# Performance work log

Hardware: AMD Instinct MI355X
Metric: run time of the kernel (lower is better)

The kernel has to match this reference:

```python
import jax, jax.numpy as jnp
import numpy as np

C = 256
CQK = C // 8  # query/key channel dim from Conv3d(in, in//8, 1)


def setup_inputs() -> dict:
    key = jax.random.key(0)
    ks = jax.random.split(key, 8)
    B, D, H, W = 2, 16, 16, 16
    x = jax.random.normal(ks[0], (B, C, D, H, W), dtype=jnp.float32)
    s = 1.0 / np.sqrt(C)
    q_w = jax.random.normal(ks[1], (CQK, C), dtype=jnp.float32) * s
    q_b = jax.random.normal(ks[2], (CQK,), dtype=jnp.float32) * 0.01
    k_w = jax.random.normal(ks[3], (CQK, C), dtype=jnp.float32) * s
    k_b = jax.random.normal(ks[4], (CQK,), dtype=jnp.float32) * 0.01
    v_w = jax.random.normal(ks[5], (C, C), dtype=jnp.float32) * s
    v_b = jax.random.normal(ks[6], (C,), dtype=jnp.float32) * 0.01
    gamma = jax.random.normal(ks[7], (1,), dtype=jnp.float32)
    return {"x": x, "q_w": q_w, "q_b": q_b, "k_w": k_w, "k_b": k_b,
            "v_w": v_w, "v_b": v_b, "gamma": gamma}


def reference(x, q_w, q_b, k_w, k_b, v_w, v_b, gamma):
    B, Cc, D, H, W = x.shape
    N = D * H * W
    xf = x.reshape(B, Cc, N)  # [B, C, N]
    # 1x1x1 Conv3d == channel-mixing matmul
    q = jnp.einsum('oc,bcn->bon', q_w, xf) + q_b[None, :, None]  # [B, C/8, N]
    k = jnp.einsum('oc,bcn->bon', k_w, xf) + k_b[None, :, None]  # [B, C/8, N]
    v = jnp.einsum('oc,bcn->bon', v_w, xf) + v_b[None, :, None]  # [B, C, N]
    # attention[b, i, j] = sum_c q[b, c, i] * k[b, c, j]
    attn = jnp.einsum('bci,bcj->bij', q, k)  # [B, N, N]
    attn = jax.nn.softmax(attn, axis=-1)
    # out[b, c, i] = sum_j v[b, c, j] * attn[b, i, j]
    out = jnp.einsum('bcj,bij->bci', v, attn)  # [B, C, N]
    out = out.reshape(B, Cc, D, H, W)
    return gamma[0] * out + x
```

## Files before the change

kernel.cpp:

```cpp
#include <hip/hip_runtime.h>

#define C_DIM 256
#define CQK   32
#define N_DIM 4096
#define B_DIM 2

typedef __attribute__((ext_vector_type(8))) short bf16x8;
typedef __attribute__((ext_vector_type(4))) float f32x4;

__device__ __forceinline__ unsigned short f2bf(float f) {
    union { float f; unsigned u; } v; v.f = f;
    unsigned r = v.u + 0x7FFFu + ((v.u >> 16) & 1u);
    return (unsigned short)(r >> 16);
}
__device__ __forceinline__ unsigned pk2(float a, float b) {
    return (unsigned)f2bf(a) | ((unsigned)f2bf(b) << 16);
}
__device__ __forceinline__ unsigned pk2t(float a, float b) {
    union { float f; unsigned u; } ua, ub; ua.f = a; ub.f = b;
    return __builtin_amdgcn_perm(ub.u, ua.u, 0x07060302u);
}
#define EXP2(x) __builtin_amdgcn_exp2f(x)
#define MFMA(A, B, C) __builtin_amdgcn_mfma_f32_16x16x32_bf16((A), (B), (C), 0, 0, 0)

__global__ __launch_bounds__(256) void wconv(
    const float* __restrict__ q_w, const float* __restrict__ q_b,
    const float* __restrict__ k_w, const float* __restrict__ k_b,
    const float* __restrict__ v_w, const float* __restrict__ v_b,
    unsigned short* __restrict__ wbf, float* __restrict__ biasf)
{
    const float LOG2E = 1.4426950408889634f;
    int o = blockIdx.x, c = threadIdx.x;
    float w;
    if (o < 32)       w = q_w[o * C_DIM + c] * LOG2E;
    else if (o < 64)  w = k_w[(o - 32) * C_DIM + c];
    else              w = v_w[(o - 64) * C_DIM + c];
    wbf[o * C_DIM + c] = f2bf(w);
    if (c == 0) biasf[o] = (o < 32) ? q_b[o] * LOG2E
                         : (o < 64) ? k_b[o - 32] : v_b[o - 64];
}

__global__ __launch_bounds__(256, 2) void qkv_proj(
    const float* __restrict__ x, const unsigned short* __restrict__ wbf,
    const float* __restrict__ biasf,
    unsigned short* __restrict__ qT, unsigned short* __restrict__ kT,
    unsigned short* __restrict__ vbf)
{
    __shared__ __align__(16) unsigned short xsT[16 * 264];
    __shared__ __align__(16) unsigned short qkbuf[2][16 * 36];
    __shared__ __align__(16) unsigned short vbb[256 * 20];
    const int t  = threadIdx.x;
    const int b  = blockIdx.x >> 8;
    const int n0 = (blockIdx.x & 255) * 16;

    {
        int n4 = t & 3, cq = t >> 2;
        const float* xp = x + ((size_t)(b * C_DIM + cq * 4)) * N_DIM + n0 + n4 * 4;
        float4 r0 = *(const float4*)xp;
        float4 r1 = *(const float4*)(xp + N_DIM);
        float4 r2 = *(const float4*)(xp + 2 * N_DIM);
        float4 r3 = *(const float4*)(xp + 3 * N_DIM);
        float a0[4], a1[4], a2[4], a3[4];
        *(float4*)a0 = r0; *(float4*)a1 = r1; *(float4*)a2 = r2; *(float4*)a3 = r3;
        #pragma unroll
        for (int k = 0; k < 4; ++k) {
            uint2 pw;
            pw.x = pk2(a0[k], a1[k]);
            pw.y = pk2(a2[k], a3[k]);
            *(uint2*)&xsT[(n4 * 4 + k) * 264 + cq * 4] = pw;
        }
    }
    __syncthreads();

    const int w = t >> 6, lid = t & 63, lr = lid & 15, lq = lid >> 4;
    f32x4 acc[5] = {};
    #pragma unroll
    for (int ks = 0; ks < 8; ++ks) {
        bf16x8 xb = *(const bf16x8*)&xsT[lr * 264 + ks * 32 + lq * 8];
        #pragma unroll
        for (int u = 0; u < 5; ++u) {
            int gm = w * 5 + u;
            bf16x8 af = *(const bf16x8*)&wbf[(gm * 16 + lr) * C_DIM + ks * 32 + lq * 8];
            acc[u] = MFMA(af, xb, acc[u]);
        }
    }
    #pragma unroll
    for (int u = 0; u < 5; ++u) {
        int gm = w * 5 + u;
        float bv[4];
        *(float4*)bv = *(const float4*)&biasf[gm * 16 + lq * 4];
        if (gm >= 4) {
            int vc = (gm - 4) * 16 + lq * 4;
            #pragma unroll
            for (int r = 0; r < 4; ++r)
                vbb[(vc + r) * 20 + lr] = f2bf(acc[u][r] + bv[r]);
        } else {
            int sel = gm >> 1, half = gm & 1;
            uint2 pw;
            pw.x = pk2(acc[u][0] + bv[0], acc[u][1] + bv[1]);
            pw.y = pk2(acc[u][2] + bv[2], acc[u][3] + bv[3]);
            *(uint2*)&qkbuf[sel][lr * 36 + half * 16 + lq * 4] = pw;
        }
    }
    __syncthreads();
    if (t < 128) {
        int sel = t >> 6, idx = t & 63;
        int n = idx >> 2, ch8 = (idx & 3) * 8;
        const unsigned short* src = &qkbuf[sel][n * 36 + ch8];
        uint2 a = *(const uint2*)src;
        uint2 c = *(const uint2*)(src + 4);
        unsigned short* dst = (sel ? kT : qT) + ((size_t)b * N_DIM + n0 + n) * CQK + ch8;
        uint4 st; st.x = a.x; st.y = a.y; st.z = c.x; st.w = c.y;
        *(uint4*)dst = st;
    }
    {
        const unsigned short* src = &vbb[t * 20];
        uint2 a = *(const uint2*)(src + 0);
        uint2 bq = *(const uint2*)(src + 4);
        uint2 c = *(const uint2*)(src + 8);
        uint2 d = *(const uint2*)(src + 12);
        unsigned short* dst = vbf +
            ((((size_t)(b * 4 + (t >> 6)) * 128 + (n0 >> 5)) * 64 + (t & 63)) * 32
             + (n0 & 31));
        uint4 s0; s0.x = a.x; s0.y = a.y; s0.z = bq.x; s0.w = bq.y;
        uint4 s1; s1.x = c.x; s1.y = c.y; s1.z = d.x; s1.w = d.y;
        *(uint4*)dst = s0;
        *(uint4*)(dst + 8) = s1;
    }
}

__global__ __launch_bounds__(256, 2) void attn_kernel(
    const unsigned short* __restrict__ qT, const unsigned short* __restrict__ kT,
    const unsigned short* __restrict__ vbf, const float* __restrict__ x,
    const float* __restrict__ gamma, float* __restrict__ out)
{
    __shared__ __align__(16) char smem[40960 + 1536];
    unsigned short* pbase = (unsigned short*)smem;
    float* obuf = (float*)smem;
    float* lbuf = (float*)(smem + 40960);

    const int t  = threadIdx.x;
    const int g  = blockIdx.x & 7;
    const int qt = blockIdx.x >> 3;
    const int b  = g >> 2;
    const int cs = g & 3;
    const int i0 = qt * 64;
    const int w = t >> 6, lid = t & 63, lr = lid & 15, lq = lid >> 4;

    const unsigned short* qTb = qT + (size_t)b * N_DIM * CQK;
    const unsigned short* kTb = kT + (size_t)b * N_DIM * CQK;
    const unsigned short* vtb = vbf + (size_t)(b * 4 + cs) * 128 * 2048;

    unsigned short* pW0 = pbase + (w * 2 + 0) * (64 * 40);
    unsigned short* pW1 = pbase + (w * 2 + 1) * (64 * 40);

    bf16x8 bq[4];
    #pragma unroll
    for (int it = 0; it < 4; ++it)
        bq[it] = *(const bf16x8*)&qTb[(i0 + it * 16 + lr) * CQK + lq * 8];

    f32x4 oa[4][4] = {};
    float lp[4] = {};

    const int jwbase = w * 1024;
    const int vlane = lr * 32 + lq * 8;

    bf16x8 akc0 = *(const bf16x8*)&kTb[(jwbase + lr) * CQK + lq * 8];
    bf16x8 akc1 = *(const bf16x8*)&kTb[(jwbase + 16 + lr) * CQK + lq * 8];
    bf16x8 avU[4];

    {
        const unsigned short* vt0 = vtb + (size_t)(w * 32) * 2048;
        #pragma unroll
        for (int ct = 0; ct < 4; ++ct)
            avU[ct] = *(const bf16x8*)&vt0[ct * 512 + vlane];
        bf16x8 akn0 = *(const bf16x8*)&kTb[(jwbase + 32 + lr) * CQK + lq * 8];
        bf16x8 akn1 = *(const bf16x8*)&kTb[(jwbase + 32 + 16 + lr) * CQK + lq * 8];
        const f32x4 z = {};
        #pragma unroll
        for (int it = 0; it < 4; ++it) {
            f32x4 s0 = MFMA(akc0, bq[it], z);
            f32x4 s1 = MFMA(akc1, bq[it], z);
            float e0 = EXP2(s0[0]), e1 = EXP2(s0[1]), e2 = EXP2(s0[2]), e3 = EXP2(s0[3]);
            float f0 = EXP2(s1[0]), f1 = EXP2(s1[1]), f2 = EXP2(s1[2]), f3 = EXP2(s1[3]);
            lp[it] += ((e0 + e1) + (e2 + e3)) + ((f0 + f1) + (f2 + f3));
            uint2 pw0; pw0.x = pk2t(e0, e1); pw0.y = pk2t(e2, e3);
            uint2 pw1; pw1.x = pk2t(f0, f1); pw1.y = pk2t(f2, f3);
            unsigned short* prow = pW0 + (it * 16 + lr) * 40;
            *(uint2*)&prow[lq * 4]      = pw0;
            *(uint2*)&prow[16 + lq * 4] = pw1;
        }
        akc0 = akn0; akc1 = akn1;
    }

    #pragma unroll 2
    for (int k = 1; k < 32; ++k) {
        const int jn = jwbase + ((k + 1) & 31) * 32;
        const unsigned short* vtk = vtb + (size_t)(w * 32 + k) * 2048;
        bf16x8 avI[4];
        #pragma unroll
        for (int ct = 0; ct < 4; ++ct)
            avI[ct] = *(const bf16x8*)&vtk[ct * 512 + vlane];
        bf16x8 akn0 = *(const bf16x8*)&kTb[(jn + lr) * CQK + lq * 8];
        bf16x8 akn1 = *(const bf16x8*)&kTb[(jn + 16 + lr) * CQK + lq * 8];
        const unsigned short* pR = (k & 1) ? pW0 : pW1;
        bf16x8 bp[4];
        #pragma unroll
        for (int it = 0; it < 4; ++it)
            bp[it] = *(const bf16x8*)&pR[(it * 16 + lr) * 40 + lq * 8];
        const f32x4 z = {};
        f32x4 s[4][2];
        #pragma unroll
        for (int it = 0; it < 4; ++it) {
            s[it][0] = MFMA(akc0, bq[it], z);
            s[it][1] = MFMA(akc1, bq[it], z);
        }
        #pragma unroll
        for (int it = 0; it < 4; ++it)
            #pragma unroll
            for (int ct = 0; ct < 4; ++ct)
                oa[ct][it] = MFMA(avU[ct], bp[it], oa[ct][it]);
        unsigned short* pWc = (k & 1) ? pW1 : pW0;
        #pragma unroll
        for (int it = 0; it < 4; ++it) {
            float e0 = EXP2(s[it][0][0]), e1 = EXP2(s[it][0][1]);
            float e2 = EXP2(s[it][0][2]), e3 = EXP2(s[it][0][3]);
            float f0 = EXP2(s[it][1][0]), f1 = EXP2(s[it][1][1]);
            float f2 = EXP2(s[it][1][2]), f3 = EXP2(s[it][1][3]);
            lp[it] += ((e0 + e1) + (e2 + e3)) + ((f0 + f1) + (f2 + f3));
            uint2 pw0; pw0.x = pk2t(e0, e1); pw0.y = pk2t(e2, e3);
            uint2 pw1; pw1.x = pk2t(f0, f1); pw1.y = pk2t(f2, f3);
            unsigned short* prow = pWc + (it * 16 + lr) * 40;
            *(uint2*)&prow[lq * 4]      = pw0;
            *(uint2*)&prow[16 + lq * 4] = pw1;
        }
        akc0 = akn0; akc1 = akn1;
        #pragma unroll
        for (int ct = 0; ct < 4; ++ct) avU[ct] = avI[ct];
    }

    {
        bf16x8 bp[4];
        #pragma unroll
        for (int it = 0; it < 4; ++it)
            bp[it] = *(const bf16x8*)&pW1[(it * 16 + lr) * 40 + lq * 8];
        #pragma unroll
        for (int it = 0; it < 4; ++it)
            #pragma unroll
            for (int ct = 0; ct < 4; ++ct)
                oa[ct][it] = MFMA(avU[ct], bp[it], oa[ct][it]);
    }

    #pragma unroll
    for (int it = 0; it < 4; ++it) {
        lp[it] += __shfl_xor(lp[it], 16);
        lp[it] += __shfl_xor(lp[it], 32);
    }
    if (lq == 0) {
        #pragma unroll
        for (int it = 0; it < 4; ++it)
            lbuf[w * 64 + it * 16 + lr] = lp[it];
    }
    __syncthreads();

    for (int ph = 0; ph < 4; ++ph) {
        if (w == ph) {
            #pragma unroll
            for (int ct = 0; ct < 4; ++ct)
                #pragma unroll
                for (int it = 0; it < 4; ++it)
                    #pragma unroll
                    for (int r = 0; r < 4; ++r) {
                        int addr = (ct * 16 + lq * 4 + r) * 68 + it * 16 + lr;
                        if (ph == 0) obuf[addr]  = oa[ct][it][r];
                        else         obuf[addr] += oa[ct][it][r];
                    }
        }
        __syncthreads();
    }
    if (t < 64) {
        float l = lbuf[t] + lbuf[64 + t] + lbuf[128 + t] + lbuf[192 + t];
        lbuf[256 + t] = 1.f / l;
    }
    __syncthreads();

    const float g2 = gamma[0];
    const int c0 = cs * 64;
    const int cc = t >> 2;
    const int ic = (t & 3) * 16;
    const size_t rowbase = ((size_t)b * C_DIM + c0 + cc) * N_DIM + i0 + ic;
    #pragma unroll
    for (int k = 0; k < 4; ++k) {
        float4 ov4 = *(const float4*)&obuf[cc * 68 + ic + k * 4];
        float4 li  = *(const float4*)&lbuf[256 + ic + k * 4];
        float4 xv  = *(const float4*)(x + rowbase + k * 4);
        float4 ov;
        ov.x = g2 * ov4.x * li.x + xv.x;
        ov.y = g2 * ov4.y * li.y + xv.y;
        ov.z = g2 * ov4.z * li.z + xv.z;
        ov.w = g2 * ov4.w * li.w + xv.w;
        *(float4*)(out + rowbase + k * 4) = ov;
    }
}

extern "C" void kernel_launch(void* const* d_in, const int* in_sizes, int n_in,
                              void* d_out, int out_size, void* d_ws, size_t ws_size,
                              hipStream_t stream) {
    const float* x     = (const float*)d_in[0];
    const float* q_w   = (const float*)d_in[1];
    const float* q_b   = (const float*)d_in[2];
    const float* k_w   = (const float*)d_in[3];
    const float* k_b   = (const float*)d_in[4];
    const float* v_w   = (const float*)d_in[5];
    const float* v_b   = (const float*)d_in[6];
    const float* gamma = (const float*)d_in[7];
    float* out = (float*)d_out;

    char* ws = (char*)d_ws;
    unsigned short* qT    = (unsigned short*)(ws);
    unsigned short* kT    = (unsigned short*)(ws + 524288);
    unsigned short* vbf   = (unsigned short*)(ws + 1048576);
    unsigned short* wbf   = (unsigned short*)(ws + 5242880);
    float*          biasf = (float*)(ws + 5406720);

    hipLaunchKernelGGL(wconv, dim3(320), dim3(256), 0, stream,
                       q_w, q_b, k_w, k_b, v_w, v_b, wbf, biasf);
    hipLaunchKernelGGL(qkv_proj, dim3(B_DIM * 256), dim3(256), 0, stream,
                       x, wbf, biasf, qT, kT, vbf);
    hipLaunchKernelGGL(attn_kernel, dim3(B_DIM * 64 * 4), dim3(256), 0, stream,
                       qT, kT, vbf, x, gamma, out);
}
```

Measured before the change: 123.3 us.

## Widen qkv_proj tile to 32 positions and regroup attention block mapping

qkv_proj now handles 32 spatial positions per block instead of 16, so each loaded weight fragment feeds two MFMAs. This halves the redundant weight traffic and the block count, and V is written as full 32-element rows. The attention kernel's block index mapping changes so that adjacent blocks share the same batch and query tile across channel slices, instead of interleaving batches, which may change L2 locality for K/V reads. The cost is more registers and LDS per qkv block and fewer blocks to fill the GPU.

```diff
diff --git a/kernel.cpp b/kernel.cpp
--- a/kernel.cpp
+++ b/kernel.cpp
@@ -46,42 +46,47 @@
     unsigned short* __restrict__ qT, unsigned short* __restrict__ kT,
     unsigned short* __restrict__ vbf)
 {
-    __shared__ __align__(16) unsigned short xsT[16 * 264];
-    __shared__ __align__(16) unsigned short qkbuf[2][16 * 36];
-    __shared__ __align__(16) unsigned short vbb[256 * 20];
+    __shared__ __align__(16) unsigned short xsT[32 * 264];
+    __shared__ __align__(16) unsigned short qkbuf[2][32 * 36];
+    __shared__ __align__(16) unsigned short vbb[256 * 36];
     const int t  = threadIdx.x;
-    const int b  = blockIdx.x >> 8;
-    const int n0 = (blockIdx.x & 255) * 16;
+    const int b  = blockIdx.x >> 7;
+    const int n0 = (blockIdx.x & 127) * 32;
 
     {
         int n4 = t & 3, cq = t >> 2;
-        const float* xp = x + ((size_t)(b * C_DIM + cq * 4)) * N_DIM + n0 + n4 * 4;
-        float4 r0 = *(const float4*)xp;
-        float4 r1 = *(const float4*)(xp + N_DIM);
-        float4 r2 = *(const float4*)(xp + 2 * N_DIM);
-        float4 r3 = *(const float4*)(xp + 3 * N_DIM);
-        float a0[4], a1[4], a2[4], a3[4];
-        *(float4*)a0 = r0; *(float4*)a1 = r1; *(float4*)a2 = r2; *(float4*)a3 = r3;
-        #pragma unroll
-        for (int k = 0; k < 4; ++k) {
+        const float* xp = x + ((size_t)(b * C_DIM + cq * 4)) * N_DIM + n0 + n4 * 8;
+        float a0[8], a1[8], a2[8], a3[8];
+        *(float4*)(a0)     = *(const float4*)(xp);
+        *(float4*)(a0 + 4) = *(const float4*)(xp + 4);
+        *(float4*)(a1)     = *(const float4*)(xp + N_DIM);
+        *(float4*)(a1 + 4) = *(const float4*)(xp + N_DIM + 4);
+        *(float4*)(a2)     = *(const float4*)(xp + 2 * N_DIM);
+        *(float4*)(a2 + 4) = *(const float4*)(xp + 2 * N_DIM + 4);
+        *(float4*)(a3)     = *(const float4*)(xp + 3 * N_DIM);
+        *(float4*)(a3 + 4) = *(const float4*)(xp + 3 * N_DIM + 4);
+        #pragma unroll
+        for (int k = 0; k < 8; ++k) {
             uint2 pw;
             pw.x = pk2(a0[k], a1[k]);
             pw.y = pk2(a2[k], a3[k]);
-            *(uint2*)&xsT[(n4 * 4 + k) * 264 + cq * 4] = pw;
+            *(uint2*)&xsT[(n4 * 8 + k) * 264 + cq * 4] = pw;
         }
     }
     __syncthreads();
 
     const int w = t >> 6, lid = t & 63, lr = lid & 15, lq = lid >> 4;
-    f32x4 acc[5] = {};
+    f32x4 acc[5][2] = {};
     #pragma unroll
     for (int ks = 0; ks < 8; ++ks) {
-        bf16x8 xb = *(const bf16x8*)&xsT[lr * 264 + ks * 32 + lq * 8];
+        bf16x8 xb0 = *(const bf16x8*)&xsT[lr * 264 + ks * 32 + lq * 8];
+        bf16x8 xb1 = *(const bf16x8*)&xsT[(16 + lr) * 264 + ks * 32 + lq * 8];
         #pragma unroll
         for (int u = 0; u < 5; ++u) {
             int gm = w * 5 + u;
             bf16x8 af = *(const bf16x8*)&wbf[(gm * 16 + lr) * C_DIM + ks * 32 + lq * 8];
-            acc[u] = MFMA(af, xb, acc[u]);
+            acc[u][0] = MFMA(af, xb0, acc[u][0]);
+            acc[u][1] = MFMA(af, xb1, acc[u][1]);
         }
     }
     #pragma unroll
@@ -89,22 +94,25 @@
         int gm = w * 5 + u;
         float bv[4];
         *(float4*)bv = *(const float4*)&biasf[gm * 16 + lq * 4];
-        if (gm >= 4) {
-            int vc = (gm - 4) * 16 + lq * 4;
-            #pragma unroll
-            for (int r = 0; r < 4; ++r)
-                vbb[(vc + r) * 20 + lr] = f2bf(acc[u][r] + bv[r]);
-        } else {
-            int sel = gm >> 1, half = gm & 1;
-            uint2 pw;
-            pw.x = pk2(acc[u][0] + bv[0], acc[u][1] + bv[1]);
-            pw.y = pk2(acc[u][2] + bv[2], acc[u][3] + bv[3]);
-            *(uint2*)&qkbuf[sel][lr * 36 + half * 16 + lq * 4] = pw;
+        #pragma unroll
+        for (int nh = 0; nh < 2; ++nh) {
+            if (gm >= 4) {
+                int vc = (gm - 4) * 16 + lq * 4;
+                #pragma unroll
+                for (int r = 0; r < 4; ++r)
+                    vbb[(vc + r) * 36 + nh * 16 + lr] = f2bf(acc[u][nh][r] + bv[r]);
+            } else {
+                int sel = gm >> 1, half = gm & 1;
+                uint2 pw;
+                pw.x = pk2(acc[u][nh][0] + bv[0], acc[u][nh][1] + bv[1]);
+                pw.y = pk2(acc[u][nh][2] + bv[2], acc[u][nh][3] + bv[3]);
+                *(uint2*)&qkbuf[sel][(nh * 16 + lr) * 36 + half * 16 + lq * 4] = pw;
+            }
         }
     }
     __syncthreads();
-    if (t < 128) {
-        int sel = t >> 6, idx = t & 63;
+    {
+        int sel = t >> 7, idx = t & 127;
         int n = idx >> 2, ch8 = (idx & 3) * 8;
         const unsigned short* src = &qkbuf[sel][n * 36 + ch8];
         uint2 a = *(const uint2*)src;
@@ -114,18 +122,25 @@
         *(uint4*)dst = st;
     }
     {
-        const unsigned short* src = &vbb[t * 20];
+        const unsigned short* src = &vbb[t * 36];
         uint2 a = *(const uint2*)(src + 0);
         uint2 bq = *(const uint2*)(src + 4);
         uint2 c = *(const uint2*)(src + 8);
         uint2 d = *(const uint2*)(src + 12);
+        uint2 e = *(const uint2*)(src + 16);
+        uint2 f = *(const uint2*)(src + 20);
+        uint2 g = *(const uint2*)(src + 24);
+        uint2 h = *(const uint2*)(src + 28);
         unsigned short* dst = vbf +
-            ((((size_t)(b * 4 + (t >> 6)) * 128 + (n0 >> 5)) * 64 + (t & 63)) * 32
-             + (n0 & 31));
+            (((size_t)(b * 4 + (t >> 6)) * 128 + (n0 >> 5)) * 64 + (t & 63)) * 32;
         uint4 s0; s0.x = a.x; s0.y = a.y; s0.z = bq.x; s0.w = bq.y;
         uint4 s1; s1.x = c.x; s1.y = c.y; s1.z = d.x; s1.w = d.y;
-        *(uint4*)dst = s0;
-        *(uint4*)(dst + 8) = s1;
+        uint4 s2; s2.x = e.x; s2.y = e.y; s2.z = f.x; s2.w = f.y;
+        uint4 s3; s3.x = g.x; s3.y = g.y; s3.z = h.x; s3.w = h.y;
+        *(uint4*)(dst)      = s0;
+        *(uint4*)(dst + 8)  = s1;
+        *(uint4*)(dst + 16) = s2;
+        *(uint4*)(dst + 24) = s3;
     }
 }
 
@@ -140,10 +155,9 @@
     float* lbuf = (float*)(smem + 40960);
 
     const int t  = threadIdx.x;
-    const int g  = blockIdx.x & 7;
-    const int qt = blockIdx.x >> 3;
-    const int b  = g >> 2;
-    const int cs = g & 3;
+    const int b  = blockIdx.x >> 8;
+    const int qt = (blockIdx.x >> 2) & 63;
+    const int cs = blockIdx.x & 3;
     const int i0 = qt * 64;
     const int w = t >> 6, lid = t & 63, lr = lid & 15, lq = lid >> 4;
 
@@ -325,7 +339,7 @@
 
     hipLaunchKernelGGL(wconv, dim3(320), dim3(256), 0, stream,
                        q_w, q_b, k_w, k_b, v_w, v_b, wbf, biasf);
-    hipLaunchKernelGGL(qkv_proj, dim3(B_DIM * 256), dim3(256), 0, stream,
+    hipLaunchKernelGGL(qkv_proj, dim3(B_DIM * 128), dim3(256), 0, stream,
                        x, wbf, biasf, qT, kT, vbf);
     hipLaunchKernelGGL(attn_kernel, dim3(B_DIM * 64 * 4), dim3(256), 0, stream,
                        qT, kT, vbf, x, gamma, out);
```

After: 120.4 us. 1.02x faster.
